# Optimization experiments

Measured on AMD Instinct MI355X. Metric: run time of the kernel, lower is better.

Reference implementation:

```python
import jax, jax.numpy as jnp
import numpy as np

# ---- module constants (from init_kwargs) ----
N_POLES = 80          # N -> dictionary width 2N+1 = 161
T_SEQ = 36            # T
LAM_F = 0.1           # lam_f
RMIN, RMAX = 0.8, 1.1 # r_r
TMIN, TMAX = 0.1, np.pi  # r_t
NSAMPLE, DDATA = 128, 50
MAX_ITER = 100


def real_D(T, rho, theta):
    # CONSTR=True path: clamp poles into the valid annulus/sector
    rho = jnp.clip(rho, RMIN, RMAX)
    theta = jnp.clip(theta, TMIN, TMAX)
    i = jnp.arange(T, dtype=rho.dtype)[:, None]            # [T,1]
    p = jnp.power(rho[None, :], i)                          # [T,N] rho^i
    W1 = p * jnp.cos(i * theta[None, :])                    # [T,N]
    W2 = p * jnp.sin(i * theta[None, :])                    # [T,N]
    ones = jnp.ones((T, 1), dtype=rho.dtype)
    return jnp.concatenate([ones, W1, W2], axis=1)          # [T, 2N+1]


def fista_reweighted(D, Y, lambd, w, max_iter=MAX_ITER):
    # D: [T,Np], Y: [n,T,d], w: [n,Np,d]
    Np = D.shape[1]
    DtD = D.T @ D                                           # [Np,Np]
    DtY = jnp.einsum('tp,ntd->npd', D, Y)                   # [n,Np,d]
    L = jnp.linalg.norm(DtD, ord=2)                         # spectral norm
    Linv = 1.0 / L
    wl = w * (lambd * Linv)
    A = jnp.eye(Np, dtype=D.dtype) - DtD * Linv             # [Np,Np]
    c_minus = DtY * Linv - wl
    c_plus = DtY * Linv + wl
    x0 = jnp.zeros_like(DtY)

    def step(carry, _):
        x, y, t, done = carry
        Ay = jnp.einsum('pq,nqd->npd', A, y)
        # soft-threshold via max/min split (as in source)
        x_new = jnp.maximum(Ay + c_minus, 0.0) + jnp.minimum(Ay + c_plus, 0.0)
        t_new = (1.0 + jnp.sqrt(1.0 + 4.0 * t * t)) / 2.0
        tt = (t - 1.0) / t_new
        y_new = x_new + tt * (x_new - x)
        conv = jnp.linalg.norm(x - x_new) / Np < 1e-5       # global check
        x_o = jnp.where(done, x, x_new)
        y_o = jnp.where(done, y, y_new)
        t_o = jnp.where(done, t, t_new)
        return (x_o, y_o, t_o, done | conv), None

    step = jax.checkpoint(step)
    init = (x0, x0, jnp.asarray(1.0, D.dtype), jnp.asarray(False))
    (x, _, _, _), _ = jax.lax.scan(step, init, None, length=max_iter)
    return x


def rh_fista(D, Y, lam):
    Np = D.shape[1]
    w = jnp.ones((Y.shape[0], Np, Y.shape[2]), dtype=Y.dtype)
    C = None
    for _ in range(2):  # fixed 2 reweighting rounds, as in source
        C = fista_reweighted(D, Y, lam, w)
        w_raw = 1.0 / (jnp.abs(C) + 0.01)
        w = w_raw / jnp.sum(jnp.abs(w_raw), axis=1, keepdims=True) * Np
    R = jnp.einsum('tp,npd->ntd', D, C)
    return C, D, R


def setup_inputs() -> dict:
    key = jax.random.key(0)
    k1, k2, k3 = jax.random.split(key, 3)
    x = jax.random.normal(k1, (NSAMPLE, T_SEQ, DDATA), dtype=jnp.float32)
    rho = jax.random.uniform(k2, (N_POLES,), dtype=jnp.float32) * (RMAX - RMIN) + RMIN
    theta = jax.random.uniform(k3, (N_POLES,), dtype=jnp.float32) * (TMAX - TMIN) + TMIN
    return {"x": x, "rho": rho, "theta": theta}


def reference(x, rho, theta):
    D = real_D(T_SEQ, rho, theta)            # [T, 2N+1]
    C, D, R = rh_fista(D, x, LAM_F)          # wiRH=True path
    return C, D, R
```

## Files before the change

### kernel.cpp

```cpp
#include <hip/hip_runtime.h>
#include <math.h>

#define NPOLES 80
#define NP 161
#define NPAD 164
#define TSEQ 36
#define NSAMP 128
#define DDATA 50
#define LAMF 0.1f
#define NPD (NP*DDATA)
#define TD (TSEQ*DDATA)
#define CSIZE (NSAMP*NPD)
#define RSIZE (NSAMP*TD)
#define DSIZE (TSEQ*NP)

#define RT_N 11
#define KC_N 5
#define FRAG_CHUNK 512

#define YBUF 10240

typedef __attribute__((ext_vector_type(8))) short s8b;
typedef __attribute__((ext_vector_type(4))) float f4;

struct u2x2 { uint2 a, b; };

__device__ __forceinline__ unsigned short f2b(float f) {
    unsigned u = __float_as_uint(f);
    unsigned r = (u + 0x7FFFu + ((u >> 16) & 1u)) >> 16;
    return (unsigned short)r;
}
__device__ __forceinline__ float b2f(unsigned short h) {
    return __uint_as_float(((unsigned)h) << 16);
}

__global__ void k_build_D(const float* __restrict__ rho, const float* __restrict__ theta,
                          float* __restrict__ Dw, float* __restrict__ Dout) {
    int idx = blockIdx.x * 256 + threadIdx.x;
    if (idx >= DSIZE) return;
    int t = idx / NP, p = idx - (idx / NP) * NP;
    float v;
    if (p == 0) {
        v = 1.f;
    } else {
        int j = (p <= NPOLES) ? (p - 1) : (p - 1 - NPOLES);
        float r  = fminf(fmaxf(rho[j],   0.8f), 1.1f);
        float th = fminf(fmaxf(theta[j], 0.1f), 3.14159265358979323846f);
        double pw  = pow((double)r, (double)t);
        double ang = (double)t * (double)th;
        v = (float)(pw * ((p <= NPOLES) ? cos(ang) : sin(ang)));
    }
    Dw[idx] = v;
    Dout[idx] = v;
}

__global__ void k_ddt(const float* __restrict__ Dw, float* __restrict__ DDt) {
    int idx = blockIdx.x * 256 + threadIdx.x;
    if (idx >= TSEQ * TSEQ) return;
    int i = idx / TSEQ, j = idx - (idx / TSEQ) * TSEQ;
    float acc = 0.f;
    for (int p = 0; p < NP; ++p) acc = fmaf(Dw[i * NP + p], Dw[j * NP + p], acc);
    DDt[idx] = acc;
}

__global__ void k_power(const float* __restrict__ DDt, float* __restrict__ scal,
                        float* __restrict__ ttab) {
    __shared__ float sM[TSEQ * TSEQ];
    __shared__ float sv[TSEQ];
    int tid = threadIdx.x;
    if (tid == 0) {
        float t = 1.f;
        for (int k = 0; k < 100; ++k) {
            float tn = (1.f + sqrtf(fmaf(4.f * t, t, 1.f))) * 0.5f;
            ttab[k] = (t - 1.f) / tn;
            t = tn;
        }
    }
    for (int i = tid; i < TSEQ * TSEQ; i += 64) sM[i] = DDt[i];
    if (tid < TSEQ) sv[tid] = 1.f;
    __syncthreads();
    for (int it = 0; it < 150; ++it) {
        float u = 0.f;
        if (tid < TSEQ) {
            for (int q = 0; q < TSEQ; ++q) u = fmaf(sM[tid * TSEQ + q], sv[q], u);
        }
        float nn = u * u;
        for (int o = 32; o > 0; o >>= 1) nn += __shfl_down(nn, o);
        nn = __shfl(nn, 0);
        float inv = rsqrtf(nn);
        __syncthreads();
        if (tid < TSEQ) sv[tid] = u * inv;
        __syncthreads();
    }
    float rq = 0.f;
    if (tid < TSEQ) {
        float uu = 0.f;
        for (int q = 0; q < TSEQ; ++q) uu = fmaf(sM[tid * TSEQ + q], sv[q], uu);
        rq = uu * sv[tid];
    }
    for (int o = 32; o > 0; o >>= 1) rq += __shfl_down(rq, o);
    if (tid == 0) { scal[0] = 1.f / rq; scal[1] = rq; }
}

__global__ void k_A(const float* __restrict__ Dw, const float* __restrict__ scal,
                    float* __restrict__ Apad) {
    int idx = blockIdx.x * 256 + threadIdx.x;
    if (idx >= NP * NPAD) return;
    int q = idx / NPAD, p = idx - (idx / NPAD) * NPAD;
    float v = 0.f;
    if (p < NP) {
        float acc = 0.f;
        for (int t = 0; t < TSEQ; ++t) acc = fmaf(Dw[t * NP + q], Dw[t * NP + p], acc);
        v = ((p == q) ? 1.f : 0.f) - acc * scal[0];
    }
    Apad[idx] = v;
}

__global__ void k_dty(const float* __restrict__ Dw, const float* __restrict__ Y,
                      float* __restrict__ dty) {
    int idx = blockIdx.x * 256 + threadIdx.x;
    if (idx >= CSIZE) return;
    int n = idx / NPD;
    int r = idx - n * NPD;
    int p = r / DDATA;
    int d = r - p * DDATA;
    const float* yp = Y + n * TD + d;
    float acc = 0.f;
    for (int t = 0; t < TSEQ; ++t) acc = fmaf(Dw[t * NP + p], yp[t * DDATA], acc);
    dty[idx] = acc;
}

__global__ void k_Afrag(const float* __restrict__ Apad,
                        short* __restrict__ AfH, short* __restrict__ AfL) {
    int idx = blockIdx.x * 256 + threadIdx.x;
    if (idx >= RT_N * KC_N * 64) return;
    int lane = idx & 63;
    int chunk = idx >> 6;
    int kc = chunk % KC_N;
    int rt = chunk / KC_N;
    int p = rt * 16 + (lane & 15);
    int q0 = kc * 32 + (lane >> 4) * 8;
    int base = chunk * FRAG_CHUNK + lane * 8;
#pragma unroll
    for (int j = 0; j < 8; ++j) {
        int q = q0 + j;
        float v = (p < NP && q < NP) ? Apad[q * NPAD + p] : 0.f;
        unsigned short h = f2b(v);
        float rem = v - b2f(h);
        AfH[base + j] = (short)h;
        AfL[base + j] = (short)f2b(rem);
    }
}

__global__ __launch_bounds__(256, 2) void k_fista(
    const float* __restrict__ Apad,
    const s8b* __restrict__ AfH, const s8b* __restrict__ AfL,
    const float* __restrict__ dty_g, const float* __restrict__ scal,
    const float* __restrict__ ttab, float* __restrict__ Cout)
{
    __shared__ char Yb[2 * YBUF];
    __shared__ float yremf[2][16];
    __shared__ float colpart[4][16];
    __shared__ float sS[16];

    const int tid = threadIdx.x;
    const int n  = blockIdx.x >> 2;
    const int dq = blockIdx.x & 3;
    const int w = tid >> 6;
    const int lane = tid & 63;
    const int c0 = lane & 15;
    const int g = lane >> 4;
    const int rt0 = w * 3;
    const int ntr = (w == 3) ? 2 : 3;
    const int ncol = (dq == 3) ? 11 : 13;
    const int colv = dq * 13 + c0;
    const bool cvalid = c0 < ncol;
    const float Linv = scal[0];
    const float lamL = LAMF * Linv;

    const int rdbase = (c0 << 3) + (g << 9);
    const int wrbase = (c0 << 3);

    s8b ahr[3][KC_N], alr[3][KC_N];
    const s8b zer = {0, 0, 0, 0, 0, 0, 0, 0};
#pragma unroll
    for (int rr = 0; rr < 3; ++rr) {
#pragma unroll
        for (int kc = 0; kc < KC_N; ++kc) {
            if (rr < ntr) {
                int ck = (rt0 + rr) * KC_N + kc;
                ahr[rr][kc] = AfH[ck * 64 + lane];
                alr[rr][kc] = AfL[ck * 64 + lane];
            } else {
                ahr[rr][kc] = zer;
                alr[rr][kc] = zer;
            }
        }
    }

    int rowb[3];
    float dtL[3][4];
    f4 a160r[3];
#pragma unroll
    for (int rr = 0; rr < 3; ++rr) {
        rowb[rr] = (rt0 + rr) * 16 + g * 4;
#pragma unroll
        for (int r = 0; r < 4; ++r) {
            int row = rowb[rr] + r;
            float v = 0.f;
            if ((rr < ntr) && row < NP && cvalid)
                v = dty_g[n * NPD + row * DDATA + colv];
            dtL[rr][r] = v * Linv;
            a160r[rr][r] = ((rr < ntr) && row < NP) ? Apad[160 * NPAD + row] : 0.f;
        }
    }

    float x_[3][4], wlam_[3][4];
#pragma unroll
    for (int rr = 0; rr < 3; ++rr)
#pragma unroll
        for (int r = 0; r < 4; ++r) wlam_[rr][r] = lamL;

#pragma unroll 1
    for (int round = 0; round < 2; ++round) {
#pragma unroll
        for (int rr = 0; rr < 3; ++rr)
#pragma unroll
            for (int r = 0; r < 4; ++r) x_[rr][r] = 0.f;
        {
            unsigned* pz = (unsigned*)Yb;
            for (int i = tid; i < YBUF / 4; i += 256) pz[i] = 0u;
            if (tid < 16) yremf[0][tid] = 0.f;
        }
        int cur = 0;
        __syncthreads();

#pragma unroll 1
        for (int it = 0; it < 100; ++it) {
            const float ttc = ttab[it];
            const int nxt = cur ^ 1;
            const char* rp = Yb + cur * YBUF + rdbase;
            char* wp = Yb + nxt * YBUF + wrbase;

            f4 acc[3];
#pragma unroll
            for (int rr = 0; rr < 3; ++rr)
#pragma unroll
                for (int r = 0; r < 4; ++r) acc[rr][r] = dtL[rr][r];

            __builtin_amdgcn_s_setprio(1);
#pragma unroll
            for (int kc = 0; kc < KC_N; ++kc) {
                const char* p = rp + kc * 2048;
                u2x2 hh2, ll2;
                hh2.a = *(const uint2*)(p);
                hh2.b = *(const uint2*)(p + 256);
                ll2.a = *(const uint2*)(p + 128);
                ll2.b = *(const uint2*)(p + 384);
                s8b bh = __builtin_bit_cast(s8b, hh2);
                s8b bl = __builtin_bit_cast(s8b, ll2);
#pragma unroll
                for (int rr = 0; rr < 3; ++rr) {
                    if (rr < ntr) {
                        acc[rr] = __builtin_amdgcn_mfma_f32_16x16x32_bf16(ahr[rr][kc], bh, acc[rr], 0, 0, 0);
                        acc[rr] = __builtin_amdgcn_mfma_f32_16x16x32_bf16(ahr[rr][kc], bl, acc[rr], 0, 0, 0);
                        acc[rr] = __builtin_amdgcn_mfma_f32_16x16x32_bf16(alr[rr][kc], bh, acc[rr], 0, 0, 0);
                    }
                }
            }
            {
                float yv = yremf[cur][c0];
#pragma unroll
                for (int rr = 0; rr < 3; ++rr)
                    if (rr < ntr)
#pragma unroll
                        for (int r = 0; r < 4; ++r)
                            acc[rr][r] = fmaf(a160r[rr][r], yv, acc[rr][r]);
            }
            __builtin_amdgcn_s_setprio(0);

#pragma unroll
            for (int rr = 0; rr < 3; ++rr) {
                if (rr < ntr) {
                    unsigned yb4[4], rb4[4];
                    float yn0 = 0.f;
#pragma unroll
                    for (int r = 0; r < 4; ++r) {
                        float bb = acc[rr][r];
                        float wl = wlam_[rr][r];
                        float cl = fminf(fmaxf(bb, -wl), wl);
                        float xn = bb - cl;
                        float yn = fmaf(ttc, xn - x_[rr][r], xn);
                        x_[rr][r] = xn;
                        if (r == 0) yn0 = yn;
                        unsigned u = __float_as_uint(yn);
                        yb4[r] = u;
                        rb4[r] = __float_as_uint(yn - __uint_as_float(u & 0xFFFF0000u));
                    }
                    int rt = rt0 + rr;
                    if (rt < 10) {
                        uint2 hp, lp;
                        hp.x = __builtin_amdgcn_perm(yb4[1], yb4[0], 0x07060302u);
                        hp.y = __builtin_amdgcn_perm(yb4[3], yb4[2], 0x07060302u);
                        lp.x = __builtin_amdgcn_perm(rb4[1], rb4[0], 0x07060302u);
                        lp.y = __builtin_amdgcn_perm(rb4[3], rb4[2], 0x07060302u);
                        char* q = wp + (rt * 4 + g) * 256;
                        *(uint2*)(q)       = hp;
                        *(uint2*)(q + 128) = lp;
                    } else if (g == 0) {
                        yremf[nxt][c0] = yn0;
                    }
                }
            }
            __syncthreads();
            cur = nxt;
        }

        if (round == 0) {
            float ps = 0.f;
#pragma unroll
            for (int rr = 0; rr < 3; ++rr) {
                if (rr < ntr) {
#pragma unroll
                    for (int r = 0; r < 4; ++r) {
                        if (rowb[rr] + r < NP)
                            ps += 1.f / (fabsf(x_[rr][r]) + 0.01f);
                    }
                }
            }
            ps += __shfl_xor(ps, 16);
            ps += __shfl_xor(ps, 32);
            if (lane < 16) colpart[w][lane] = ps;
            __syncthreads();
            if (tid < 16) {
                float s = colpart[0][tid] + colpart[1][tid] + colpart[2][tid] + colpart[3][tid];
                sS[tid] = (float)NP / s;
            }
            __syncthreads();
            float sc = sS[c0] * lamL;
#pragma unroll
            for (int rr = 0; rr < 3; ++rr)
#pragma unroll
                for (int r = 0; r < 4; ++r)
                    wlam_[rr][r] = (1.f / (fabsf(x_[rr][r]) + 0.01f)) * sc;
            __syncthreads();
        }
    }

#pragma unroll
    for (int rr = 0; rr < 3; ++rr) {
        if ((rr < ntr) && cvalid) {
#pragma unroll
            for (int r = 0; r < 4; ++r) {
                int row = rowb[rr] + r;
                if (row < NP)
                    Cout[n * NPD + row * DDATA + colv] = x_[rr][r];
            }
        }
    }
}

__global__ void k_R(const float* __restrict__ Dw, const float* __restrict__ Cf,
                    float* __restrict__ Rout) {
    int idx = blockIdx.x * 256 + threadIdx.x;
    if (idx >= RSIZE) return;
    int n = idx / TD;
    int r = idx - n * TD;
    int t = r / DDATA;
    int d = r - t * DDATA;
    const float* xp = Cf + n * NPD + d;
    float acc = 0.f;
    for (int p = 0; p < NP; ++p) acc = fmaf(Dw[t * NP + p], xp[p * DDATA], acc);
    Rout[idx] = acc;
}

extern "C" void kernel_launch(void* const* d_in, const int* in_sizes, int n_in,
                              void* d_out, int out_size, void* d_ws, size_t ws_size,
                              hipStream_t stream) {
    const float* Y     = (const float*)d_in[0];
    const float* rho   = (const float*)d_in[1];
    const float* theta = (const float*)d_in[2];
    float* Cout = (float*)d_out;
    float* Dout = Cout + CSIZE;
    float* Rout = Dout + DSIZE;

    float* ws    = (float*)d_ws;
    float* Dw    = ws;
    float* Apad  = Dw + 5824;
    float* DDt   = Apad + 26416;
    float* scal  = DDt + 1312;
    float* ttabd = scal + 16;
    float* dty   = ttabd + 112;
    float* AfH_f = dty + CSIZE;
    float* AfL_f = AfH_f + 14080;

    k_build_D<<<(DSIZE + 255) / 256, 256, 0, stream>>>(rho, theta, Dw, Dout);
    k_ddt<<<(TSEQ * TSEQ + 255) / 256, 256, 0, stream>>>(Dw, DDt);
    k_power<<<1, 64, 0, stream>>>(DDt, scal, ttabd);
    k_A<<<(NP * NPAD + 255) / 256, 256, 0, stream>>>(Dw, scal, Apad);
    k_dty<<<(CSIZE + 255) / 256, 256, 0, stream>>>(Dw, Y, dty);
    k_Afrag<<<(RT_N * KC_N * 64 + 255) / 256, 256, 0, stream>>>(Apad, (short*)AfH_f, (short*)AfL_f);

    k_fista<<<NSAMP * 4, 256, 0, stream>>>(Apad, (const s8b*)AfH_f, (const s8b*)AfL_f,
                                           dty, scal, ttabd, Cout);

    k_R<<<(RSIZE + 255) / 256, 256, 0, stream>>>(Dw, Cout, Rout);
}
```

Measured before the change: 392.2 us.

## Fuse setup kernels into one prep kernel and fold DtY and R into FISTA

Merges D construction, DDt, the spectral-norm estimate, A construction and fragment packing into one single-block prep kernel. The power iteration becomes repeated matrix squaring with max-normalisation followed by a Rayleigh quotient. DtY is now computed inside the FISTA kernel from Y, and the reconstruction R is computed at the end of FISTA from shared memory. This removes six kernel launches and the global round trips for dty and C. In exchange the prep work runs serially on one block, which may lengthen the critical path, and the squaring method could change L slightly.

After: 459.8 us. 17.2% more time.

```diff
diff --git a/kernel.cpp b/kernel.cpp
--- a/kernel.cpp
+++ b/kernel.cpp
@@ -34,40 +34,21 @@
     return __uint_as_float(((unsigned)h) << 16);
 }
 
-__global__ void k_build_D(const float* __restrict__ rho, const float* __restrict__ theta,
-                          float* __restrict__ Dw, float* __restrict__ Dout) {
-    int idx = blockIdx.x * 256 + threadIdx.x;
-    if (idx >= DSIZE) return;
-    int t = idx / NP, p = idx - (idx / NP) * NP;
-    float v;
-    if (p == 0) {
-        v = 1.f;
-    } else {
-        int j = (p <= NPOLES) ? (p - 1) : (p - 1 - NPOLES);
-        float r  = fminf(fmaxf(rho[j],   0.8f), 1.1f);
-        float th = fminf(fmaxf(theta[j], 0.1f), 3.14159265358979323846f);
-        double pw  = pow((double)r, (double)t);
-        double ang = (double)t * (double)th;
-        v = (float)(pw * ((p <= NPOLES) ? cos(ang) : sin(ang)));
-    }
-    Dw[idx] = v;
-    Dout[idx] = v;
-}
-
-__global__ void k_ddt(const float* __restrict__ Dw, float* __restrict__ DDt) {
-    int idx = blockIdx.x * 256 + threadIdx.x;
-    if (idx >= TSEQ * TSEQ) return;
-    int i = idx / TSEQ, j = idx - (idx / TSEQ) * TSEQ;
-    float acc = 0.f;
-    for (int p = 0; p < NP; ++p) acc = fmaf(Dw[i * NP + p], Dw[j * NP + p], acc);
-    DDt[idx] = acc;
-}
-
-__global__ void k_power(const float* __restrict__ DDt, float* __restrict__ scal,
-                        float* __restrict__ ttab) {
-    __shared__ float sM[TSEQ * TSEQ];
-    __shared__ float sv[TSEQ];
-    int tid = threadIdx.x;
+__global__ __launch_bounds__(256) void k_prep(
+    const float* __restrict__ rho, const float* __restrict__ theta,
+    float* __restrict__ Dw, float* __restrict__ Dout, float* __restrict__ Apad,
+    float* __restrict__ scal, float* __restrict__ ttab,
+    short* __restrict__ AfH, short* __restrict__ AfL)
+{
+    __shared__ float sD[TSEQ][NP];
+    __shared__ float sM[1296];
+    __shared__ float sB0[1296];
+    __shared__ float sB1[1296];
+    __shared__ float sred[256];
+    __shared__ float sv[40];
+    __shared__ float sLinv;
+    const int tid = threadIdx.x;
+
     if (tid == 0) {
         float t = 1.f;
         for (int k = 0; k < 100; ++k) {
@@ -76,89 +57,139 @@
             t = tn;
         }
     }
-    for (int i = tid; i < TSEQ * TSEQ; i += 64) sM[i] = DDt[i];
-    if (tid < TSEQ) sv[tid] = 1.f;
-    __syncthreads();
-    for (int it = 0; it < 150; ++it) {
+
+    for (int idx = tid; idx < DSIZE; idx += 256) {
+        int t = idx / NP, p = idx - (idx / NP) * NP;
+        float v;
+        if (p == 0) {
+            v = 1.f;
+        } else {
+            int j = (p <= NPOLES) ? (p - 1) : (p - 1 - NPOLES);
+            float r  = fminf(fmaxf(rho[j],   0.8f), 1.1f);
+            float th = fminf(fmaxf(theta[j], 0.1f), 3.14159265358979323846f);
+            double pw  = pow((double)r, (double)t);
+            double ang = (double)t * (double)th;
+            v = (float)(pw * ((p <= NPOLES) ? cos(ang) : sin(ang)));
+        }
+        sD[t][p] = v;
+        Dw[idx] = v;
+        Dout[idx] = v;
+    }
+    __syncthreads();
+
+    for (int idx = tid; idx < 1296; idx += 256) {
+        int i = idx / 36, j = idx - (idx / 36) * 36;
+        float acc = 0.f;
+        for (int p = 0; p < NP; ++p) acc = fmaf(sD[i][p], sD[j][p], acc);
+        sM[idx] = acc;
+    }
+    __syncthreads();
+
+    {
+        float mx = 0.f;
+        for (int idx = tid; idx < 1296; idx += 256) mx = fmaxf(mx, fabsf(sM[idx]));
+        sred[tid] = mx;
+        __syncthreads();
+        for (int s = 128; s > 0; s >>= 1) {
+            if (tid < s) sred[tid] = fmaxf(sred[tid], sred[tid + s]);
+            __syncthreads();
+        }
+        float inv = 1.f / sred[0];
+        for (int idx = tid; idx < 1296; idx += 256) sB0[idx] = sM[idx] * inv;
+    }
+    __syncthreads();
+
+    float* bs = sB0;
+    float* bd = sB1;
+    for (int sq = 0; sq < 8; ++sq) {
+        for (int idx = tid; idx < 1296; idx += 256) {
+            int i = idx / 36, j = idx - (idx / 36) * 36;
+            float acc = 0.f;
+            for (int k2 = 0; k2 < 36; ++k2) acc = fmaf(bs[i * 36 + k2], bs[k2 * 36 + j], acc);
+            bd[idx] = acc;
+        }
+        __syncthreads();
+        float m2 = 0.f;
+        for (int idx = tid; idx < 1296; idx += 256) m2 = fmaxf(m2, fabsf(bd[idx]));
+        sred[tid] = m2;
+        __syncthreads();
+        for (int s = 128; s > 0; s >>= 1) {
+            if (tid < s) sred[tid] = fmaxf(sred[tid], sred[tid + s]);
+            __syncthreads();
+        }
+        float inv = 1.f / sred[0];
+        for (int idx = tid; idx < 1296; idx += 256) bd[idx] *= inv;
+        __syncthreads();
+        float* tmp = bs; bs = bd; bd = tmp;
+    }
+
+    if (tid < 36) {
+        float s = 0.f;
+        for (int k2 = 0; k2 < 36; ++k2) s += bs[tid * 36 + k2];
+        sv[tid] = s;
+    }
+    __syncthreads();
+    if (tid < 36) {
         float u = 0.f;
-        if (tid < TSEQ) {
-            for (int q = 0; q < TSEQ; ++q) u = fmaf(sM[tid * TSEQ + q], sv[q], u);
-        }
-        float nn = u * u;
-        for (int o = 32; o > 0; o >>= 1) nn += __shfl_down(nn, o);
-        nn = __shfl(nn, 0);
-        float inv = rsqrtf(nn);
-        __syncthreads();
-        if (tid < TSEQ) sv[tid] = u * inv;
-        __syncthreads();
-    }
-    float rq = 0.f;
-    if (tid < TSEQ) {
-        float uu = 0.f;
-        for (int q = 0; q < TSEQ; ++q) uu = fmaf(sM[tid * TSEQ + q], sv[q], uu);
-        rq = uu * sv[tid];
-    }
-    for (int o = 32; o > 0; o >>= 1) rq += __shfl_down(rq, o);
-    if (tid == 0) { scal[0] = 1.f / rq; scal[1] = rq; }
+        for (int k2 = 0; k2 < 36; ++k2) u = fmaf(sM[tid * 36 + k2], sv[k2], u);
+        sred[tid] = u * sv[tid];
+        sred[40 + tid] = sv[tid] * sv[tid];
+    }
+    __syncthreads();
+    if (tid == 0) {
+        float num = 0.f, den = 0.f;
+        for (int i = 0; i < 36; ++i) { num += sred[i]; den += sred[40 + i]; }
+        float L = num / den;
+        scal[0] = 1.f / L; scal[1] = L;
+        sLinv = 1.f / L;
+    }
+    __syncthreads();
+    const float Linv = sLinv;
+
+    for (int idx = tid; idx < NP * NPAD; idx += 256) {
+        int q = idx / NPAD, p = idx - (idx / NPAD) * NPAD;
+        float v = 0.f;
+        if (p < NP) {
+            float acc = 0.f;
+            for (int t = 0; t < TSEQ; ++t) acc = fmaf(sD[t][q], sD[t][p], acc);
+            v = ((p == q) ? 1.f : 0.f) - acc * Linv;
+        }
+        Apad[idx] = v;
+    }
+
+    for (int idx = tid; idx < RT_N * KC_N * 64; idx += 256) {
+        int lane = idx & 63;
+        int chunk = idx >> 6;
+        int kc = chunk % KC_N;
+        int rt = chunk / KC_N;
+        int p = rt * 16 + (lane & 15);
+        int q0 = kc * 32 + (lane >> 4) * 8;
+        int base = chunk * FRAG_CHUNK + lane * 8;
+#pragma unroll
+        for (int j = 0; j < 8; ++j) {
+            int q = q0 + j;
+            float v = 0.f;
+            if (p < NP && q < NP) {
+                float acc = 0.f;
+                for (int t = 0; t < TSEQ; ++t) acc = fmaf(sD[t][q], sD[t][p], acc);
+                v = ((p == q) ? 1.f : 0.f) - acc * Linv;
+            }
+            unsigned short h = f2b(v);
+            float rem = v - b2f(h);
+            AfH[base + j] = (short)h;
+            AfL[base + j] = (short)f2b(rem);
+        }
+    }
 }
 
-__global__ void k_A(const float* __restrict__ Dw, const float* __restrict__ scal,
-                    float* __restrict__ Apad) {
-    int idx = blockIdx.x * 256 + threadIdx.x;
-    if (idx >= NP * NPAD) return;
-    int q = idx / NPAD, p = idx - (idx / NPAD) * NPAD;
-    float v = 0.f;
-    if (p < NP) {
-        float acc = 0.f;
-        for (int t = 0; t < TSEQ; ++t) acc = fmaf(Dw[t * NP + q], Dw[t * NP + p], acc);
-        v = ((p == q) ? 1.f : 0.f) - acc * scal[0];
-    }
-    Apad[idx] = v;
-}
-
-__global__ void k_dty(const float* __restrict__ Dw, const float* __restrict__ Y,
-                      float* __restrict__ dty) {
-    int idx = blockIdx.x * 256 + threadIdx.x;
-    if (idx >= CSIZE) return;
-    int n = idx / NPD;
-    int r = idx - n * NPD;
-    int p = r / DDATA;
-    int d = r - p * DDATA;
-    const float* yp = Y + n * TD + d;
-    float acc = 0.f;
-    for (int t = 0; t < TSEQ; ++t) acc = fmaf(Dw[t * NP + p], yp[t * DDATA], acc);
-    dty[idx] = acc;
-}
-
-__global__ void k_Afrag(const float* __restrict__ Apad,
-                        short* __restrict__ AfH, short* __restrict__ AfL) {
-    int idx = blockIdx.x * 256 + threadIdx.x;
-    if (idx >= RT_N * KC_N * 64) return;
-    int lane = idx & 63;
-    int chunk = idx >> 6;
-    int kc = chunk % KC_N;
-    int rt = chunk / KC_N;
-    int p = rt * 16 + (lane & 15);
-    int q0 = kc * 32 + (lane >> 4) * 8;
-    int base = chunk * FRAG_CHUNK + lane * 8;
-#pragma unroll
-    for (int j = 0; j < 8; ++j) {
-        int q = q0 + j;
-        float v = (p < NP && q < NP) ? Apad[q * NPAD + p] : 0.f;
-        unsigned short h = f2b(v);
-        float rem = v - b2f(h);
-        AfH[base + j] = (short)h;
-        AfL[base + j] = (short)f2b(rem);
-    }
-}
-
 __global__ __launch_bounds__(256, 2) void k_fista(
+    const float* __restrict__ Y, const float* __restrict__ Dw,
     const float* __restrict__ Apad,
     const s8b* __restrict__ AfH, const s8b* __restrict__ AfL,
-    const float* __restrict__ dty_g, const float* __restrict__ scal,
-    const float* __restrict__ ttab, float* __restrict__ Cout)
+    const float* __restrict__ scal, const float* __restrict__ ttab,
+    float* __restrict__ Cout, float* __restrict__ Rout)
 {
-    __shared__ char Yb[2 * YBUF];
+    __shared__ __align__(16) char Yb[2 * YBUF];
     __shared__ float yremf[2][16];
     __shared__ float colpart[4][16];
     __shared__ float sS[16];
@@ -208,8 +239,11 @@
         for (int r = 0; r < 4; ++r) {
             int row = rowb[rr] + r;
             float v = 0.f;
-            if ((rr < ntr) && row < NP && cvalid)
-                v = dty_g[n * NPD + row * DDATA + colv];
+            if ((rr < ntr) && row < NP && cvalid) {
+                const float* yp = Y + n * TD + colv;
+                for (int t = 0; t < TSEQ; ++t)
+                    v = fmaf(Dw[t * NP + row], yp[t * DDATA], v);
+            }
             dtL[rr][r] = v * Linv;
             a160r[rr][r] = ((rr < ntr) && row < NP) ? Apad[160 * NPAD + row] : 0.f;
         }
@@ -358,20 +392,30 @@
             }
         }
     }
-}
-
-__global__ void k_R(const float* __restrict__ Dw, const float* __restrict__ Cf,
-                    float* __restrict__ Rout) {
-    int idx = blockIdx.x * 256 + threadIdx.x;
-    if (idx >= RSIZE) return;
-    int n = idx / TD;
-    int r = idx - n * TD;
-    int t = r / DDATA;
-    int d = r - t * DDATA;
-    const float* xp = Cf + n * NPD + d;
-    float acc = 0.f;
-    for (int p = 0; p < NP; ++p) acc = fmaf(Dw[t * NP + p], xp[p * DDATA], acc);
-    Rout[idx] = acc;
+
+    {
+        float* xs = (float*)Yb;
+        __syncthreads();
+#pragma unroll
+        for (int rr = 0; rr < 3; ++rr) {
+            if (rr < ntr) {
+#pragma unroll
+                for (int r = 0; r < 4; ++r)
+                    xs[(rowb[rr] + r) * 16 + c0] = x_[rr][r];
+            }
+        }
+        __syncthreads();
+        for (int o = tid; o < TSEQ * 13; o += 256) {
+            int t = o / 13, c = o - (o / 13) * 13;
+            int cg = dq * 13 + c;
+            if (cg < DDATA) {
+                float acc = 0.f;
+                for (int p = 0; p < NP; ++p)
+                    acc = fmaf(Dw[t * NP + p], xs[p * 16 + c], acc);
+                Rout[n * TD + t * DDATA + cg] = acc;
+            }
+        }
+    }
 }
 
 extern "C" void kernel_launch(void* const* d_in, const int* in_sizes, int n_in,
@@ -387,22 +431,15 @@
     float* ws    = (float*)d_ws;
     float* Dw    = ws;
     float* Apad  = Dw + 5824;
-    float* DDt   = Apad + 26416;
-    float* scal  = DDt + 1312;
+    float* scal  = Apad + 26416;
     float* ttabd = scal + 16;
-    float* dty   = ttabd + 112;
-    float* AfH_f = dty + CSIZE;
+    float* AfH_f = ttabd + 112;
     float* AfL_f = AfH_f + 14080;
 
-    k_build_D<<<(DSIZE + 255) / 256, 256, 0, stream>>>(rho, theta, Dw, Dout);
-    k_ddt<<<(TSEQ * TSEQ + 255) / 256, 256, 0, stream>>>(Dw, DDt);
-    k_power<<<1, 64, 0, stream>>>(DDt, scal, ttabd);
-    k_A<<<(NP * NPAD + 255) / 256, 256, 0, stream>>>(Dw, scal, Apad);
-    k_dty<<<(CSIZE + 255) / 256, 256, 0, stream>>>(Dw, Y, dty);
-    k_Afrag<<<(RT_N * KC_N * 64 + 255) / 256, 256, 0, stream>>>(Apad, (short*)AfH_f, (short*)AfL_f);
-
-    k_fista<<<NSAMP * 4, 256, 0, stream>>>(Apad, (const s8b*)AfH_f, (const s8b*)AfL_f,
-                                           dty, scal, ttabd, Cout);
-
-    k_R<<<(RSIZE + 255) / 256, 256, 0, stream>>>(Dw, Cout, Rout);
+    k_prep<<<1, 256, 0, stream>>>(rho, theta, Dw, Dout, Apad, scal, ttabd,
+                                  (short*)AfH_f, (short*)AfL_f);
+
+    k_fista<<<NSAMP * 4, 256, 0, stream>>>(Y, Dw, Apad,
+                                           (const s8b*)AfH_f, (const s8b*)AfL_f,
+                                           scal, ttabd, Cout, Rout);
 }
```

## Replace power iteration with repeated matrix squaring for spectral norm

Applied to the files above, without the earlier changes.

Swaps the 150-step serial power iteration on the 36x36 Gram matrix for 8 rounds of matrix squaring (M^256), renormalising by the max entry after each round, then takes a Rayleigh quotient from the row sums. The kernel now runs with 256 threads instead of 64. The aim is to shorten the long serial chain of tiny matvecs and barriers in this single-block kernel. In exchange it adds O(n^3) work per squaring and more barriers per round, and convergence depends on the eigenvalue gap reached after 256 effective iterations.

New measurement: 370.9 us. 1.06x faster.

```diff
diff --git a/kernel.cpp b/kernel.cpp
--- a/kernel.cpp
+++ b/kernel.cpp
@@ -63,11 +63,16 @@
     DDt[idx] = acc;
 }
 
-__global__ void k_power(const float* __restrict__ DDt, float* __restrict__ scal,
-                        float* __restrict__ ttab) {
-    __shared__ float sM[TSEQ * TSEQ];
-    __shared__ float sv[TSEQ];
-    int tid = threadIdx.x;
+__global__ __launch_bounds__(256) void k_power2(const float* __restrict__ DDt,
+                                                float* __restrict__ scal,
+                                                float* __restrict__ ttab) {
+    __shared__ float sM[1296];
+    __shared__ float sB0[1296];
+    __shared__ float sB1[1296];
+    __shared__ float sred[256];
+    __shared__ float sv[40];
+    const int tid = threadIdx.x;
+
     if (tid == 0) {
         float t = 1.f;
         for (int k = 0; k < 100; ++k) {
@@ -76,30 +81,67 @@
             t = tn;
         }
     }
-    for (int i = tid; i < TSEQ * TSEQ; i += 64) sM[i] = DDt[i];
-    if (tid < TSEQ) sv[tid] = 1.f;
+
+    for (int i = tid; i < 1296; i += 256) sM[i] = DDt[i];
     __syncthreads();
-    for (int it = 0; it < 150; ++it) {
+
+    {
+        float mx = 0.f;
+        for (int idx = tid; idx < 1296; idx += 256) mx = fmaxf(mx, fabsf(sM[idx]));
+        sred[tid] = mx;
+        __syncthreads();
+        for (int s = 128; s > 0; s >>= 1) {
+            if (tid < s) sred[tid] = fmaxf(sred[tid], sred[tid + s]);
+            __syncthreads();
+        }
+        float inv = 1.f / sred[0];
+        for (int idx = tid; idx < 1296; idx += 256) sB0[idx] = sM[idx] * inv;
+    }
+    __syncthreads();
+
+    float* bs = sB0;
+    float* bd = sB1;
+    for (int sq = 0; sq < 8; ++sq) {
+        for (int idx = tid; idx < 1296; idx += 256) {
+            int i = idx / 36, j = idx - (idx / 36) * 36;
+            float acc = 0.f;
+            for (int k2 = 0; k2 < 36; ++k2) acc = fmaf(bs[i * 36 + k2], bs[k2 * 36 + j], acc);
+            bd[idx] = acc;
+        }
+        __syncthreads();
+        float m2 = 0.f;
+        for (int idx = tid; idx < 1296; idx += 256) m2 = fmaxf(m2, fabsf(bd[idx]));
+        sred[tid] = m2;
+        __syncthreads();
+        for (int s = 128; s > 0; s >>= 1) {
+            if (tid < s) sred[tid] = fmaxf(sred[tid], sred[tid + s]);
+            __syncthreads();
+        }
+        float inv = 1.f / sred[0];
+        for (int idx = tid; idx < 1296; idx += 256) bd[idx] *= inv;
+        __syncthreads();
+        float* tmp = bs; bs = bd; bd = tmp;
+    }
+
+    if (tid < 36) {
+        float s = 0.f;
+        for (int k2 = 0; k2 < 36; ++k2) s += bs[tid * 36 + k2];
+        sv[tid] = s;
+    }
+    __syncthreads();
+    if (tid < 36) {
         float u = 0.f;
-        if (tid < TSEQ) {
-            for (int q = 0; q < TSEQ; ++q) u = fmaf(sM[tid * TSEQ + q], sv[q], u);
-        }
-        float nn = u * u;
-        for (int o = 32; o > 0; o >>= 1) nn += __shfl_down(nn, o);
-        nn = __shfl(nn, 0);
-        float inv = rsqrtf(nn);
-        __syncthreads();
-        if (tid < TSEQ) sv[tid] = u * inv;
-        __syncthreads();
-    }
-    float rq = 0.f;
-    if (tid < TSEQ) {
-        float uu = 0.f;
-        for (int q = 0; q < TSEQ; ++q) uu = fmaf(sM[tid * TSEQ + q], sv[q], uu);
-        rq = uu * sv[tid];
-    }
-    for (int o = 32; o > 0; o >>= 1) rq += __shfl_down(rq, o);
-    if (tid == 0) { scal[0] = 1.f / rq; scal[1] = rq; }
+        for (int k2 = 0; k2 < 36; ++k2) u = fmaf(sM[tid * 36 + k2], sv[k2], u);
+        sred[tid] = u * sv[tid];
+        sred[40 + tid] = sv[tid] * sv[tid];
+    }
+    __syncthreads();
+    if (tid == 0) {
+        float num = 0.f, den = 0.f;
+        for (int i = 0; i < 36; ++i) { num += sred[i]; den += sred[40 + i]; }
+        float L = num / den;
+        scal[0] = 1.f / L; scal[1] = L;
+    }
 }
 
 __global__ void k_A(const float* __restrict__ Dw, const float* __restrict__ scal,
@@ -396,7 +438,7 @@
 
     k_build_D<<<(DSIZE + 255) / 256, 256, 0, stream>>>(rho, theta, Dw, Dout);
     k_ddt<<<(TSEQ * TSEQ + 255) / 256, 256, 0, stream>>>(Dw, DDt);
-    k_power<<<1, 64, 0, stream>>>(DDt, scal, ttabd);
+    k_power2<<<1, 256, 0, stream>>>(DDt, scal, ttabd);
     k_A<<<(NP * NPAD + 255) / 256, 256, 0, stream>>>(Dw, scal, Apad);
     k_dty<<<(CSIZE + 255) / 256, 256, 0, stream>>>(Dw, Y, dty);
     k_Afrag<<<(RT_N * KC_N * 64 + 255) / 256, 256, 0, stream>>>(Apad, (short*)AfH_f, (short*)AfL_f);
```
